# Performance work log

Hardware: AMD Instinct MI355X
Metric: run time of the kernel (lower is better)

The kernel has to match this reference:

```python
import jax, jax.numpy as jnp
import numpy as np

D_MODEL = 1024
N_HEADS = 16
D_HEAD = D_MODEL // N_HEADS
B, T = 2, 2048


def setup_inputs() -> dict:
    key = jax.random.key(0)
    ks = jax.random.split(key, 6)
    scale = 1.0 / np.sqrt(D_MODEL)
    x = jax.random.normal(ks[0], (B, T, D_MODEL), dtype=jnp.float32)
    mask = jax.random.randint(ks[1], (1, 1, T, T), 0, 2, dtype=jnp.int32)
    Wqkv = jax.random.normal(ks[2], (D_MODEL, 3 * D_MODEL), dtype=jnp.float32) * scale
    bqkv = jnp.zeros((3 * D_MODEL,), dtype=jnp.float32)
    Wproj = jax.random.normal(ks[3], (D_MODEL, D_MODEL), dtype=jnp.float32) * scale
    bproj = jnp.zeros((D_MODEL,), dtype=jnp.float32)
    return {"x": x, "mask": mask, "Wqkv": Wqkv, "bqkv": bqkv,
            "Wproj": Wproj, "bproj": bproj}


def reference(x, mask, Wqkv, bqkv, Wproj, bproj):
    Bx, Tx, C = x.shape
    qkv = x @ Wqkv + bqkv                      # [B,T,3C]
    q, k, v = jnp.split(qkv, 3, axis=-1)       # each [B,T,C]

    def heads(t):  # [B,T,C] -> [B,H,T,dh]
        return t.reshape(Bx, Tx, N_HEADS, D_HEAD).transpose(0, 2, 1, 3)

    q, k, v = heads(q), heads(k), heads(v)
    att = jnp.einsum('bhqd,bhkd->bhqk', q, k) / jnp.sqrt(jnp.float32(D_HEAD))
    att = jnp.where(mask == 1, -jnp.inf, att)
    att = jax.nn.softmax(att, axis=-1)
    out = jnp.einsum('bhqk,bhkd->bhqd', att, v)  # [B,H,T,dh]
    out = out.transpose(0, 2, 1, 3).reshape(Bx, Tx, C)
    return out @ Wproj + bproj
```

## Files before the change

### kernel.cpp

```cpp
#include <hip/hip_runtime.h>
#include <hip/hip_bf16.h>

#define T_DIM 2048
#define C_DIM 1024
#define NHEAD 16
#define DHEAD 64

typedef __attribute__((ext_vector_type(8))) short s16x8;
typedef __attribute__((ext_vector_type(4))) short s16x4;
typedef __attribute__((ext_vector_type(4))) float f32x4;
typedef __attribute__((ext_vector_type(4))) unsigned short u16x4;

typedef __attribute__((address_space(3))) unsigned short lds_us;
typedef const __attribute__((address_space(1))) void glb_v;

static __device__ __forceinline__ unsigned short f2bfu(float f){
  __hip_bfloat16 h = __float2bfloat16(f);
  unsigned short u;
  __builtin_memcpy(&u, &h, 2);
  return u;
}

static __device__ __forceinline__ f32x4 MFMA16(s16x8 a, s16x8 b, f32x4 c){
  return __builtin_amdgcn_mfma_f32_16x16x32_bf16(a, b, c, 0, 0, 0);
}

__global__ __launch_bounds__(256) void cvt_bf16_kernel(const float* __restrict__ in,
                                                       unsigned short* __restrict__ out, int n4){
  int i = blockIdx.x*256 + threadIdx.x;
  if (i < n4){
    float4 v = reinterpret_cast<const float4*>(in)[i];
    u16x4 o;
    o.x = f2bfu(v.x); o.y = f2bfu(v.y); o.z = f2bfu(v.z); o.w = f2bfu(v.w);
    reinterpret_cast<u16x4*>(out)[i] = o;
  }
}

__global__ __launch_bounds__(256) void transpose_cvt_kernel(const float* __restrict__ src,
                                                            unsigned short* __restrict__ dst,
                                                            int K, int N){
  __shared__ unsigned short tile[64][65];
  int n0 = blockIdx.x*64, k0 = blockIdx.y*64;
  int tid = threadIdx.x;
  #pragma unroll
  for (int i=0;i<16;i++){
    int e = i*256 + tid; int r = e>>6, c = e&63;
    tile[r][c] = f2bfu(src[(size_t)(k0+r)*N + n0 + c]);
  }
  __syncthreads();
  #pragma unroll
  for (int i=0;i<16;i++){
    int e = i*256 + tid; int r = e>>6, c = e&63;
    dst[(size_t)(n0+r)*K + k0 + c] = tile[c][r];
  }
}

__global__ __launch_bounds__(256) void mask_bits_kernel(const int* __restrict__ m,
                                                        unsigned int* __restrict__ bits){
  int i = blockIdx.x*256 + threadIdx.x;
  unsigned long long b = __ballot(m[i] == 1);
  int lane = threadIdx.x & 63;
  if (lane == 0)  bits[i>>5] = (unsigned int)b;
  if (lane == 32) bits[i>>5] = (unsigned int)(b>>32);
}

__global__ __launch_bounds__(256) void transpose_v_kernel(const unsigned short* __restrict__ v,
                                                          unsigned short* __restrict__ vt){
  __shared__ unsigned short tile[64][65];
  int bh = blockIdx.y;
  int t0 = blockIdx.x*64;
  const unsigned short* src = v + (size_t)bh*T_DIM*DHEAD;
  unsigned short* dst = vt + (size_t)bh*T_DIM*DHEAD;
  int tid = threadIdx.x;
  #pragma unroll
  for (int i=0;i<16;i++){
    int e = i*256+tid; int r = e>>6, c = e&63;
    tile[r][c] = src[(size_t)(t0+r)*DHEAD + c];
  }
  __syncthreads();
  #pragma unroll
  for (int i=0;i<16;i++){
    int e = i*256+tid; int r = e>>6, c = e&63;
    dst[(size_t)r*T_DIM + t0 + c] = tile[c][r];
  }
}

template<int MODE>
__global__ __launch_bounds__(256) void gemm_kernel(const unsigned short* __restrict__ A,
    const unsigned short* __restrict__ Bt, const float* __restrict__ bias,
    unsigned short* __restrict__ qo, unsigned short* __restrict__ ko,
    unsigned short* __restrict__ vo, float* __restrict__ out)
{
  const int K = 1024;
  __shared__ __align__(16) unsigned short As[128*64];
  __shared__ __align__(16) unsigned short Bs[128*64];
  int tid = threadIdx.x;
  int lane = tid & 63, wave = tid >> 6;
  int m0 = blockIdx.y*128, n0 = blockIdx.x*128;
  int wm = (wave>>1)*64, wn = (wave&1)*64;
  int lr = lane & 15, lg = lane >> 4;
  int srow  = wave*8 + (lane>>3);
  int sslot = (lane&7) ^ (lane>>3);
  const unsigned short* Asrc = A  + (size_t)(m0+srow)*K + sslot*8;
  const unsigned short* Bsrc = Bt + (size_t)(n0+srow)*K + sslot*8;
  unsigned ldsoff = (unsigned)(wave*512 + lane*8);
  f32x4 acc[4][4];
  #pragma unroll
  for (int i=0;i<4;i++){
    #pragma unroll
    for (int j=0;j<4;j++){
      #pragma unroll
      for (int r=0;r<4;r++) acc[i][j][r] = 0.f;
    }
  }
  for (int kt=0; kt<K; kt+=64){
    #pragma unroll
    for (int i=0;i<4;i++){
      __builtin_amdgcn_global_load_lds((glb_v*)(Asrc + (size_t)i*32*K + kt),
                                       (lds_us*)(As + ldsoff + i*2048), 16, 0, 0);
      __builtin_amdgcn_global_load_lds((glb_v*)(Bsrc + (size_t)i*32*K + kt),
                                       (lds_us*)(Bs + ldsoff + i*2048), 16, 0, 0);
    }
    __syncthreads();
    #pragma unroll
    for (int kk=0; kk<2; kk++){
      s16x8 av[4], bv[4];
      #pragma unroll
      for (int i=0;i<4;i++){
        av[i] = *reinterpret_cast<const s16x8*>(&As[(wm+i*16+lr)*64 + (((kk*4+lg)^(lr&7))<<3)]);
        bv[i] = *reinterpret_cast<const s16x8*>(&Bs[(wn+i*16+lr)*64 + (((kk*4+lg)^(lr&7))<<3)]);
      }
      #pragma unroll
      for (int i=0;i<4;i++){
        #pragma unroll
        for (int j=0;j<4;j++)
          acc[i][j] = MFMA16(av[i], bv[j], acc[i][j]);
      }
    }
    __syncthreads();
  }
  #pragma unroll
  for (int j=0;j<4;j++){
    int n = n0 + wn + j*16 + lr;
    float bvl = bias[n];
    #pragma unroll
    for (int i=0;i<4;i++){
      #pragma unroll
      for (int r=0;r<4;r++){
        int m = m0 + wm + i*16 + lg*4 + r;
        float val = acc[i][j][r] + bvl;
        if (MODE == 0){
          int which = n >> 10, c = n & 1023;
          int h = c >> 6, d = c & 63;
          int b = m >> 11, t = m & 2047;
          size_t idx = ((size_t)((b*NHEAD + h)*T_DIM + t))*DHEAD + d;
          unsigned short us = f2bfu(val);
          if (which == 0) qo[idx] = us;
          else if (which == 1) ko[idx] = us;
          else vo[idx] = us;
        } else {
          out[(size_t)m*C_DIM + n] = val;
        }
      }
    }
  }
}

__global__ __launch_bounds__(256) void attn_kernel(const unsigned short* __restrict__ q,
    const unsigned short* __restrict__ k, const unsigned short* __restrict__ vt,
    const unsigned int* __restrict__ mbits, unsigned short* __restrict__ aout)
{
  __shared__ __align__(16) unsigned short Ks[64*64];
  __shared__ __align__(16) unsigned short Vs[64*64];
  __shared__ __align__(16) unsigned short Ps[4][16][72];
  int bh = blockIdx.y;
  int q0 = blockIdx.x*64;
  int tid = threadIdx.x, lane = tid&63, wave = tid>>6;
  int lr = lane&15, lg = lane>>4;
  const unsigned short* qp = q  + (size_t)bh*T_DIM*DHEAD;
  const unsigned short* kp = k  + (size_t)bh*T_DIM*DHEAD;
  const unsigned short* vp = vt + (size_t)bh*T_DIM*DHEAD;
  int qw = q0 + wave*16;
  s16x8 qf[2];
  #pragma unroll
  for (int kk=0;kk<2;kk++)
    qf[kk] = *reinterpret_cast<const s16x8*>(qp + (size_t)(qw+lr)*DHEAD + kk*32 + lg*8);
  int srow  = wave*8 + (lane>>3);
  int sslot = (lane&7) ^ (lane>>3);
  const unsigned short* Ksrc = kp + (size_t)srow*DHEAD + sslot*8;
  const unsigned short* Vsrc = vp + (size_t)srow*T_DIM + sslot*8;
  unsigned ldsoff = (unsigned)(wave*512 + lane*8);
  f32x4 o[4];
  #pragma unroll
  for (int cb=0;cb<4;cb++){
    #pragma unroll
    for (int r=0;r<4;r++) o[cb][r]=0.f;
  }
  const float SC = 0.125f * 1.44269504f;
  float m = -1e30f, l = 0.f;
  const unsigned int* mptr = mbits + (size_t)(qw + lr)*(T_DIM/32);

  for (int k0=0; k0<T_DIM; k0+=64){
    #pragma unroll
    for (int i=0;i<2;i++){
      __builtin_amdgcn_global_load_lds((glb_v*)(Ksrc + (size_t)(k0 + i*32)*DHEAD),
                                       (lds_us*)(Ks + ldsoff + i*2048), 16, 0, 0);
      __builtin_amdgcn_global_load_lds((glb_v*)(Vsrc + (size_t)i*32*T_DIM + k0),
                                       (lds_us*)(Vs + ldsoff + i*2048), 16, 0, 0);
    }
    __syncthreads();
    f32x4 st[4];
    #pragma unroll
    for (int cb=0;cb<4;cb++){
      f32x4 a;
      #pragma unroll
      for (int r=0;r<4;r++) a[r]=0.f;
      #pragma unroll
      for (int kk=0;kk<2;kk++){
        s16x8 kf = *reinterpret_cast<const s16x8*>(
            &Ks[(cb*16+lr)*64 + (((kk*4+lg)^(lr&7))<<3)]);
        a = MFMA16(kf, qf[kk], a);
      }
      st[cb] = a;
    }
    unsigned mw0 = mptr[(k0>>5)];
    unsigned mw1 = mptr[(k0>>5)+1];
    #pragma unroll
    for (int cb=0;cb<4;cb++){
      unsigned msel = (cb<2) ? mw0 : mw1;
      unsigned ms = msel >> ((cb&1)*16 + lg*4);
      #pragma unroll
      for (int r=0;r<4;r++){
        float val = st[cb][r]*SC;
        st[cb][r] = ((ms>>r)&1u) ? -1e30f : val;
      }
    }
    float pmax = st[0][0];
    #pragma unroll
    for (int cb=0;cb<4;cb++){
      #pragma unroll
      for (int r=0;r<4;r++) pmax = fmaxf(pmax, st[cb][r]);
    }
    pmax = fmaxf(pmax, __shfl_xor(pmax, 16));
    pmax = fmaxf(pmax, __shfl_xor(pmax, 32));
    float mnew = fmaxf(m, pmax);
    float corr = exp2f(m - mnew);
    m = mnew;
    float rs = 0.f;
    #pragma unroll
    for (int cb=0;cb<4;cb++){
      #pragma unroll
      for (int r=0;r<4;r++){
        float p = exp2f(st[cb][r] - mnew);
        st[cb][r] = p;
        rs += p;
      }
    }
    rs += __shfl_xor(rs, 16);
    rs += __shfl_xor(rs, 32);
    l = l*corr + rs;
    float corrO[4];
    #pragma unroll
    for (int r=0;r<4;r++) corrO[r] = __shfl(corr, lg*4 + r);
    #pragma unroll
    for (int cb=0;cb<4;cb++){
      #pragma unroll
      for (int r=0;r<4;r++) o[cb][r] *= corrO[r];
    }
    #pragma unroll
    for (int cb=0;cb<4;cb++){
      s16x4 pk;
      #pragma unroll
      for (int r=0;r<4;r++) pk[r] = (short)f2bfu(st[cb][r]);
      *reinterpret_cast<s16x4*>(&Ps[wave][lr][cb*16 + lg*4]) = pk;
    }
    s16x8 pf[2];
    #pragma unroll
    for (int kk=0;kk<2;kk++)
      pf[kk] = *reinterpret_cast<const s16x8*>(&Ps[wave][lr][kk*32 + lg*8]);
    #pragma unroll
    for (int cb=0;cb<4;cb++){
      #pragma unroll
      for (int kk=0;kk<2;kk++){
        s16x8 vf = *reinterpret_cast<const s16x8*>(
            &Vs[(cb*16+lr)*64 + (((kk*4+lg)^(lr&7))<<3)]);
        o[cb] = MFMA16(pf[kk], vf, o[cb]);
      }
    }
    __syncthreads();
  }
  int b = bh >> 4, h = bh & 15;
  float inv = l > 0.f ? 1.f/l : 0.f;
  #pragma unroll
  for (int r=0;r<4;r++){
    float invO = __shfl(inv, lg*4 + r);
    int row = b*T_DIM + qw + lg*4 + r;
    #pragma unroll
    for (int cb=0;cb<4;cb++){
      int d = cb*16 + lr;
      aout[(size_t)row*C_DIM + h*DHEAD + d] = f2bfu(o[cb][r]*invO);
    }
  }
}

extern "C" void kernel_launch(void* const* d_in, const int* in_sizes, int n_in,
                              void* d_out, int out_size, void* d_ws, size_t ws_size,
                              hipStream_t stream){
  const float* x     = (const float*)d_in[0];
  const int*   mask  = (const int*)d_in[1];
  const float* Wqkv  = (const float*)d_in[2];
  const float* bqkv  = (const float*)d_in[3];
  const float* Wproj = (const float*)d_in[4];
  const float* bproj = (const float*)d_in[5];
  float* out = (float*)d_out;
  char* ws = (char*)d_ws;
  const size_t MB = (size_t)1<<20;
  unsigned short* xb     = (unsigned short*)(ws + 0*MB);
  unsigned short* wqkvT  = (unsigned short*)(ws + 8*MB);
  unsigned short* wprojT = (unsigned short*)(ws + 14*MB);
  unsigned int*   mbits  = (unsigned int*)(ws + 16*MB);
  unsigned short* qb     = (unsigned short*)(ws + 17*MB);
  unsigned short* kb     = (unsigned short*)(ws + 25*MB);
  unsigned short* vb     = (unsigned short*)(ws + 33*MB);
  unsigned short* vtb    = (unsigned short*)(ws + 41*MB);
  unsigned short* aout   = xb;

  cvt_bf16_kernel<<<dim3(4096), dim3(256), 0, stream>>>(x, xb, (2*2048*1024)/4);
  transpose_cvt_kernel<<<dim3(48,16), dim3(256), 0, stream>>>(Wqkv, wqkvT, 1024, 3072);
  transpose_cvt_kernel<<<dim3(16,16), dim3(256), 0, stream>>>(Wproj, wprojT, 1024, 1024);
  mask_bits_kernel<<<dim3((2048*2048)/256), dim3(256), 0, stream>>>(mask, mbits);
  gemm_kernel<0><<<dim3(24,32), dim3(256), 0, stream>>>(xb, wqkvT, bqkv, qb, kb, vb, nullptr);
  transpose_v_kernel<<<dim3(32,32), dim3(256), 0, stream>>>(vb, vtb);
  attn_kernel<<<dim3(32,32), dim3(256), 0, stream>>>(qb, kb, vtb, mbits, aout);
  gemm_kernel<1><<<dim3(8,32), dim3(256), 0, stream>>>(aout, wprojT, bproj, nullptr, nullptr, nullptr, out);
}
```

Before: 258.6 us.

## Fold QK scale into Q projection, lazy max rescaling, MFMA row-sum

Applies the softmax scale and log2e factor to Q inside the QKV GEMM epilogue so the attention loop no longer multiplies scores. Online-softmax rescaling of the output accumulator is skipped unless the running max grows by more than 8 (in log2 units) somewhere in the wave. The row sum of probabilities is computed with an extra MFMA against a vector of ones, which replaces the shuffle-based reduction. Probabilities are packed to bf16 with v_cvt_pk_bf16_f32. In exchange each tile costs two extra MFMAs and four more accumulator registers, and the row sum is now taken from the bf16-rounded probabilities.

```diff
diff --git a/kernel.cpp b/kernel.cpp
--- a/kernel.cpp
+++ b/kernel.cpp
@@ -13,12 +13,20 @@
 
 typedef __attribute__((address_space(3))) unsigned short lds_us;
 typedef const __attribute__((address_space(1))) void glb_v;
+
+#define SC_QK (0.125f * 1.44269504f)
 
 static __device__ __forceinline__ unsigned short f2bfu(float f){
   __hip_bfloat16 h = __float2bfloat16(f);
   unsigned short u;
   __builtin_memcpy(&u, &h, 2);
   return u;
+}
+
+static __device__ __forceinline__ unsigned cvt_pk_bf16(float lo, float hi){
+  unsigned r;
+  asm("v_cvt_pk_bf16_f32 %0, %1, %2" : "=v"(r) : "v"(lo), "v"(hi));
+  return r;
 }
 
 static __device__ __forceinline__ f32x4 MFMA16(s16x8 a, s16x8 b, f32x4 c){
@@ -154,10 +162,9 @@
           int h = c >> 6, d = c & 63;
           int b = m >> 11, t = m & 2047;
           size_t idx = ((size_t)((b*NHEAD + h)*T_DIM + t))*DHEAD + d;
-          unsigned short us = f2bfu(val);
-          if (which == 0) qo[idx] = us;
-          else if (which == 1) ko[idx] = us;
-          else vo[idx] = us;
+          if (which == 0)      qo[idx] = f2bfu(val * SC_QK);
+          else if (which == 1) ko[idx] = f2bfu(val);
+          else                 vo[idx] = f2bfu(val);
         } else {
           out[(size_t)m*C_DIM + n] = val;
         }
@@ -185,19 +192,21 @@
   #pragma unroll
   for (int kk=0;kk<2;kk++)
     qf[kk] = *reinterpret_cast<const s16x8*>(qp + (size_t)(qw+lr)*DHEAD + kk*32 + lg*8);
+  s16x8 ones;
+  #pragma unroll
+  for (int j=0;j<8;j++) ones[j] = (short)0x3F80;
   int srow  = wave*8 + (lane>>3);
   int sslot = (lane&7) ^ (lane>>3);
   const unsigned short* Ksrc = kp + (size_t)srow*DHEAD + sslot*8;
   const unsigned short* Vsrc = vp + (size_t)srow*T_DIM + sslot*8;
   unsigned ldsoff = (unsigned)(wave*512 + lane*8);
-  f32x4 o[4];
-  #pragma unroll
-  for (int cb=0;cb<4;cb++){
+  f32x4 o[5];
+  #pragma unroll
+  for (int cb=0;cb<5;cb++){
     #pragma unroll
     for (int r=0;r<4;r++) o[cb][r]=0.f;
   }
-  const float SC = 0.125f * 1.44269504f;
-  float m = -1e30f, l = 0.f;
+  float m = -1e30f;
   const unsigned int* mptr = mbits + (size_t)(qw + lr)*(T_DIM/32);
 
   for (int k0=0; k0<T_DIM; k0+=64){
@@ -230,10 +239,8 @@
       unsigned msel = (cb<2) ? mw0 : mw1;
       unsigned ms = msel >> ((cb&1)*16 + lg*4);
       #pragma unroll
-      for (int r=0;r<4;r++){
-        float val = st[cb][r]*SC;
-        st[cb][r] = ((ms>>r)&1u) ? -1e30f : val;
-      }
+      for (int r=0;r<4;r++)
+        st[cb][r] = ((ms>>r)&1u) ? -1e30f : st[cb][r];
     }
     float pmax = st[0][0];
     #pragma unroll
@@ -243,36 +250,30 @@
     }
     pmax = fmaxf(pmax, __shfl_xor(pmax, 16));
     pmax = fmaxf(pmax, __shfl_xor(pmax, 32));
-    float mnew = fmaxf(m, pmax);
-    float corr = exp2f(m - mnew);
-    m = mnew;
-    float rs = 0.f;
-    #pragma unroll
-    for (int cb=0;cb<4;cb++){
-      #pragma unroll
-      for (int r=0;r<4;r++){
-        float p = exp2f(st[cb][r] - mnew);
-        st[cb][r] = p;
-        rs += p;
-      }
-    }
-    rs += __shfl_xor(rs, 16);
-    rs += __shfl_xor(rs, 32);
-    l = l*corr + rs;
-    float corrO[4];
-    #pragma unroll
-    for (int r=0;r<4;r++) corrO[r] = __shfl(corr, lg*4 + r);
-    #pragma unroll
-    for (int cb=0;cb<4;cb++){
-      #pragma unroll
-      for (int r=0;r<4;r++) o[cb][r] *= corrO[r];
-    }
-    #pragma unroll
-    for (int cb=0;cb<4;cb++){
-      s16x4 pk;
-      #pragma unroll
-      for (int r=0;r<4;r++) pk[r] = (short)f2bfu(st[cb][r]);
-      *reinterpret_cast<s16x4*>(&Ps[wave][lr][cb*16 + lg*4]) = pk;
+    if (!__all(pmax <= m + 8.0f)){
+      float mnew = fmaxf(m, pmax);
+      float corr = exp2f(m - mnew);
+      m = mnew;
+      float corrO[4];
+      #pragma unroll
+      for (int r=0;r<4;r++) corrO[r] = __shfl(corr, lg*4 + r);
+      #pragma unroll
+      for (int cb=0;cb<5;cb++){
+        #pragma unroll
+        for (int r=0;r<4;r++) o[cb][r] *= corrO[r];
+      }
+    }
+    #pragma unroll
+    for (int cb=0;cb<4;cb++){
+      #pragma unroll
+      for (int r=0;r<4;r++) st[cb][r] = exp2f(st[cb][r] - m);
+    }
+    #pragma unroll
+    for (int cb=0;cb<4;cb++){
+      uint2 w;
+      w.x = cvt_pk_bf16(st[cb][0], st[cb][1]);
+      w.y = cvt_pk_bf16(st[cb][2], st[cb][3]);
+      *reinterpret_cast<uint2*>(&Ps[wave][lr][cb*16 + lg*4]) = w;
     }
     s16x8 pf[2];
     #pragma unroll
@@ -287,13 +288,15 @@
         o[cb] = MFMA16(pf[kk], vf, o[cb]);
       }
     }
+    o[4] = MFMA16(pf[0], ones, o[4]);
+    o[4] = MFMA16(pf[1], ones, o[4]);
     __syncthreads();
   }
   int b = bh >> 4, h = bh & 15;
-  float inv = l > 0.f ? 1.f/l : 0.f;
   #pragma unroll
   for (int r=0;r<4;r++){
-    float invO = __shfl(inv, lg*4 + r);
+    float l = o[4][r];
+    float invO = l > 0.f ? 1.f/l : 0.f;
     int row = b*T_DIM + qw + lg*4 + r;
     #pragma unroll
     for (int cb=0;cb<4;cb++){
```

After: 254.0 us. Within noise of the previous version (-1.8%).
